# Performance work log

Hardware: AMD Instinct MI355X
Metric: run time of the kernel (lower is better)

Reference implementation:

```python
import jax, jax.numpy as jnp
import numpy as np
from jax import lax

D_MODEL = 64      # feature_dim
D_STATE = 16      # state_dim
D_CONV = 4        # conv_dim
EXPAND = 2
D_INNER = EXPAND * D_MODEL          # 128
DT_RANK = (D_MODEL + 15) // 16      # ceil(d_model/16) = 4, mamba default
IN_DIM = 64
LN_EPS = 1e-3                        # keras LayerNormalization default epsilon


def setup_inputs() -> dict:
    key = jax.random.key(0)
    ks = jax.random.split(key, 12)
    B, L = 16, 8192
    s = 0.02
    x = jax.random.normal(ks[0], (B, L, IN_DIM), jnp.float32)
    W_in = jax.random.normal(ks[1], (IN_DIM, D_MODEL), jnp.float32) * s
    b_in = jnp.zeros((D_MODEL,), jnp.float32)
    in_proj_w = jax.random.normal(ks[2], (D_MODEL, 2 * D_INNER), jnp.float32) * s
    conv_w = jax.random.normal(ks[3], (D_INNER, D_CONV), jnp.float32) * 0.1
    conv_b = jnp.zeros((D_INNER,), jnp.float32)
    x_proj_w = jax.random.normal(ks[4], (D_INNER, DT_RANK + 2 * D_STATE), jnp.float32) * s
    dt_proj_w = jax.random.normal(ks[5], (DT_RANK, D_INNER), jnp.float32) * (DT_RANK ** -0.5)
    # dt bias init so softplus(dt) lands roughly in [dt_min, dt_max]
    dt = jnp.exp(jax.random.uniform(ks[6], (D_INNER,)) * (np.log(0.1) - np.log(0.001)) + np.log(0.001))
    dt_proj_b = dt + jnp.log(-jnp.expm1(-dt))  # inverse softplus
    A_log = jnp.log(jnp.broadcast_to(jnp.arange(1, D_STATE + 1, dtype=jnp.float32), (D_INNER, D_STATE)))
    D_skip = jnp.ones((D_INNER,), jnp.float32)
    out_proj_w = jax.random.normal(ks[7], (D_INNER, D_MODEL), jnp.float32) * s
    ln_gamma = jnp.ones((D_MODEL,), jnp.float32)
    ln_beta = jnp.zeros((D_MODEL,), jnp.float32)
    return {"x": x, "W_in": W_in, "b_in": b_in, "in_proj_w": in_proj_w,
            "conv_w": conv_w, "conv_b": conv_b, "x_proj_w": x_proj_w,
            "dt_proj_w": dt_proj_w, "dt_proj_b": dt_proj_b, "A_log": A_log,
            "D_skip": D_skip, "out_proj_w": out_proj_w,
            "ln_gamma": ln_gamma, "ln_beta": ln_beta}


def reference(x, W_in, b_in, in_proj_w, conv_w, conv_b, x_proj_w,
              dt_proj_w, dt_proj_b, A_log, D_skip, out_proj_w, ln_gamma, ln_beta):
    B, L, _ = x.shape
    # Conv1D kernel_size=1 input projection
    xin = x @ W_in + b_in                          # [B,L,D_MODEL]
    # --- Mamba ---
    xz = xin @ in_proj_w                           # [B,L,2*D_INNER]
    xc, z = xz[..., :D_INNER], xz[..., D_INNER:]
    # causal depthwise conv (groups=d_inner, padding=d_conv-1, crop to L)
    xp = jnp.pad(xc, ((0, 0), (D_CONV - 1, 0), (0, 0)))
    xconv = conv_b
    for k in range(D_CONV):
        xconv = xconv + xp[:, k:k + L, :] * conv_w[:, k]
    u = jax.nn.silu(xconv)                         # [B,L,D_INNER]
    dbc = u @ x_proj_w                             # [B,L,DT_RANK+2*D_STATE]
    dt = jax.nn.softplus(dbc[..., :DT_RANK] @ dt_proj_w + dt_proj_b)   # [B,L,D_INNER]
    Bm = dbc[..., DT_RANK:DT_RANK + D_STATE]       # [B,L,D_STATE]
    Cm = dbc[..., DT_RANK + D_STATE:]              # [B,L,D_STATE]
    A = -jnp.exp(A_log)                            # [D_INNER,D_STATE]

    def step(h, xs):
        dt_t, b_t, c_t, u_t = xs                   # [B,Di],[B,Ds],[B,Ds],[B,Di]
        dA = jnp.exp(dt_t[:, :, None] * A)         # [B,Di,Ds]
        h = dA * h + (dt_t * u_t)[:, :, None] * b_t[:, None, :]
        y = jnp.einsum('bds,bs->bd', h, c_t)
        return h, y

    xs = (jnp.swapaxes(dt, 0, 1), jnp.swapaxes(Bm, 0, 1),
          jnp.swapaxes(Cm, 0, 1), jnp.swapaxes(u, 0, 1))
    h0 = jnp.zeros((B, D_INNER, D_STATE), x.dtype)
    _, ys = lax.scan(step, h0, xs)                 # ys: [L,B,D_INNER]
    y = jnp.swapaxes(ys, 0, 1) + u * D_skip
    y = y * jax.nn.silu(z)
    h_out = y @ out_proj_w                         # [B,L,D_MODEL]
    # residual + LayerNorm
    res = h_out + xin
    mu = jnp.mean(res, axis=-1, keepdims=True)
    var = jnp.mean(jnp.square(res - mu), axis=-1, keepdims=True)
    return ln_gamma * (res - mu) * lax.rsqrt(var + LN_EPS) + ln_beta
```

## Files before the change

kernel.cpp:

```cpp
#include <hip/hip_runtime.h>
#include <hip/hip_bf16.h>
#include <hip/hip_fp16.h>

#define B_SZ   16
#define L_SZ   8192
#define DM     64
#define DI     128
#define NCH    256
#define CLEN   32
#define CH     64
#define RT     80
#define PA     72
#define PU     136
#define PC     132
#define LN_EPS 1e-3f

typedef float  f4 __attribute__((ext_vector_type(4)));
typedef float  f2 __attribute__((ext_vector_type(2)));
typedef short  s8 __attribute__((ext_vector_type(8)));
typedef unsigned short u16;
typedef unsigned int   u32;
#define MFMA16 __builtin_amdgcn_mfma_f32_16x16x32_bf16

__device__ __forceinline__ u16 f2bfu(float f) {
    u32 u = __float_as_uint(f);
    return (u16)((u + 0x7FFFu + ((u >> 16) & 1u)) >> 16);
}
__device__ __forceinline__ u32 pk2bf(float a, float b) {
    return (u32)f2bfu(a) | ((u32)f2bfu(b) << 16);
}
__device__ __forceinline__ float bflo(u32 u) { return __uint_as_float(u << 16); }
__device__ __forceinline__ float bfhi(u32 u) { return __uint_as_float(u & 0xFFFF0000u); }
__device__ __forceinline__ float bfu2f(u16 h) { return __uint_as_float((u32)h << 16); }
__device__ __forceinline__ float h2f(u32 lo16) {
    return __half2float(__ushort_as_half((u16)(lo16 & 0xFFFFu)));
}
__device__ __forceinline__ float fsig(float v) {
    return __builtin_amdgcn_rcpf(1.f + __expf(-v));
}
__device__ __forceinline__ float fsp(float v) {
    return fmaxf(v, 0.f) + __logf(1.f + __expf(-fabsf(v)));
}

__global__ __launch_bounds__(256) void k_prep(
    const float* __restrict__ W_in, const float* __restrict__ in_proj,
    const float* __restrict__ x_proj, const float* __restrict__ Wout,
    u16* __restrict__ Wf1, u16* __restrict__ Wf2,
    u16* __restrict__ Wf3, u16* __restrict__ Wf4)
{
    const int tid = threadIdx.x;
    for (int g = tid; g < 512; g += 256) {
        int lane = g & 63, ks = (g >> 6) & 1, nt = g >> 7;
        int n = nt * 16 + (lane & 15), kb = ks * 32 + (lane >> 4) * 8;
        for (int j = 0; j < 8; j++) Wf1[g * 8 + j] = f2bfu(W_in[(kb + j) * 64 + n]);
    }
    for (int g = tid; g < 2048; g += 256) {
        int lane = g & 63, ks = (g >> 6) & 1, nt = g >> 7;
        int n = nt * 16 + (lane & 15), kb = ks * 32 + (lane >> 4) * 8;
        for (int j = 0; j < 8; j++) Wf2[g * 8 + j] = f2bfu(in_proj[(kb + j) * 256 + n]);
    }
    for (int g = tid; g < 768; g += 256) {
        int lane = g & 63, ks = (g >> 6) & 3, nt = g >> 8;
        int n = nt * 16 + (lane & 15), kb = ks * 32 + (lane >> 4) * 8;
        for (int j = 0; j < 8; j++)
            Wf3[g * 8 + j] = f2bfu(n < 36 ? x_proj[(kb + j) * 36 + n] : 0.f);
    }
    for (int g = tid; g < 1024; g += 256) {
        int lane = g & 63, ks = (g >> 6) & 3, nt = g >> 8;
        int n = nt * 16 + (lane & 15), kb = ks * 32 + (lane >> 4) * 8;
        for (int j = 0; j < 8; j++) Wf4[g * 8 + j] = f2bfu(Wout[(kb + j) * 64 + n]);
    }
}

__global__ __launch_bounds__(256, 4) void k_frontend(
    const float* __restrict__ x, const float* __restrict__ b_in,
    const float* __restrict__ conv_w, const float* __restrict__ conv_b,
    const float* __restrict__ dt_w, const float* __restrict__ dt_b,
    const u16* __restrict__ Wf1, const u16* __restrict__ Wf2, const u16* __restrict__ Wf3,
    const float* __restrict__ A_log,
    float* __restrict__ xin_g, u32* __restrict__ dtu_g,
    float* __restrict__ B_g, float* __restrict__ C_g, u16* __restrict__ sz_g,
    float* __restrict__ hl_ws, float* __restrict__ sdt_ws)
{
    __shared__ __align__(16) char sm[40736];
    u16*   smA   = (u16*)sm;
    u16*   smB   = (u16*)(sm + 11520);
    u16*   smU   = (u16*)sm;
    float* smDtr = (float*)(sm + 17408);
    float* smBf  = (float*)(sm + 18432);
    u16*   smC   = (u16*)(sm + 23040);
    u32*   smDt  = (u32*)(sm + 23040);

    const int tid = threadIdx.x;
    const int w = tid >> 6, lane = tid & 63;
    const int n16 = lane & 15, quad = lane >> 4;
    const int b = blockIdx.y, c0 = blockIdx.x * CH;
    const long long tokbase = (long long)b * L_SZ + c0;

    for (int idx = tid; idx < RT * 16; idx += 256) {
        int r = idx >> 4, c4 = idx & 15;
        int l = c0 - 3 + r;
        float4 v = make_float4(0.f, 0.f, 0.f, 0.f);
        if (r < 67 && l >= 0)
            v = *(const float4*)(x + ((long long)b * L_SZ + l) * 64 + c4 * 4);
        *(uint2*)((char*)smA + r * 144 + c4 * 8) = make_uint2(pk2bf(v.x, v.y), pk2bf(v.z, v.w));
    }
    __syncthreads();

    {
        s8 b0 = *(const s8*)(Wf1 + ((w * 2 + 0) * 64 + lane) * 8);
        s8 b1 = *(const s8*)(Wf1 + ((w * 2 + 1) * 64 + lane) * 8);
        float bias = b_in[w * 16 + n16];
        for (int m = 0; m < 5; m++) {
            int ar = m * 16 + n16;
            s8 a0 = *(const s8*)(smA + ar * PA + quad * 8);
            s8 a1 = *(const s8*)(smA + ar * PA + 32 + quad * 8);
            f4 acc = {0.f, 0.f, 0.f, 0.f};
            acc = MFMA16(a0, b0, acc, 0, 0, 0);
            acc = MFMA16(a1, b1, acc, 0, 0, 0);
#pragma unroll
            for (int reg = 0; reg < 4; reg++) {
                int rr = m * 16 + quad * 4 + reg;
                float v = acc[reg] + bias;
                smB[rr * PA + w * 16 + n16] = f2bfu(v);
                if (rr >= 3 && rr < 67)
                    xin_g[(tokbase + rr - 3) * 64 + w * 16 + n16] = v;
            }
        }
    }
    __syncthreads();

    {
        s8 bf[4][2];
#pragma unroll
        for (int i = 0; i < 4; i++)
#pragma unroll
            for (int ks = 0; ks < 2; ks++)
                bf[i][ks] = *(const s8*)(Wf2 + (((w * 4 + i) * 2 + ks) * 64 + lane) * 8);
        for (int m = 0; m < 5; m++) {
            int ar = m * 16 + n16;
            s8 a0 = *(const s8*)(smB + ar * PA + quad * 8);
            s8 a1 = *(const s8*)(smB + ar * PA + 32 + quad * 8);
#pragma unroll
            for (int i = 0; i < 4; i++) {
                f4 acc = {0.f, 0.f, 0.f, 0.f};
                acc = MFMA16(a0, bf[i][0], acc, 0, 0, 0);
                acc = MFMA16(a1, bf[i][1], acc, 0, 0, 0);
                int cg = (w * 4 + i) * 16 + n16;
#pragma unroll
                for (int reg = 0; reg < 4; reg++) {
                    int rr = m * 16 + quad * 4 + reg;
                    float v = acc[reg];
                    if (cg < 128) {
                        if (rr < 67) {
                            int l = c0 - 3 + rr;
                            smC[rr * PC + cg] = f2bfu(l >= 0 ? v : 0.f);
                        }
                    } else if (rr >= 3 && rr < 67) {
                        sz_g[(tokbase + rr - 3) * 128 + (cg - 128)] = f2bfu(v * fsig(v));
                    }
                }
            }
        }
    }
    __syncthreads();

    {
        const int d2 = lane * 2, ctb = w * 16;
        float4 cw0 = ((const float4*)conv_w)[d2];
        float4 cw1 = ((const float4*)conv_w)[d2 + 1];
        float cb0 = conv_b[d2], cb1 = conv_b[d2 + 1];
        u32 r0 = *(const u32*)((char*)smC + (ctb + 0) * 264 + lane * 4);
        u32 r1 = *(const u32*)((char*)smC + (ctb + 1) * 264 + lane * 4);
        u32 r2 = *(const u32*)((char*)smC + (ctb + 2) * 264 + lane * 4);
#pragma unroll 4
        for (int j = 0; j < 16; j++) {
            int ct = ctb + j;
            u32 r3 = *(const u32*)((char*)smC + (ct + 3) * 264 + lane * 4);
            float v0 = cb0 + bflo(r0) * cw0.x + bflo(r1) * cw0.y + bflo(r2) * cw0.z + bflo(r3) * cw0.w;
            float v1 = cb1 + bfhi(r0) * cw1.x + bfhi(r1) * cw1.y + bfhi(r2) * cw1.z + bfhi(r3) * cw1.w;
            u32 pk = pk2bf(v0 * fsig(v0), v1 * fsig(v1));
            *(u32*)(smU + ct * PU + d2) = pk;
            r0 = r1; r1 = r2; r2 = r3;
        }
    }
    __syncthreads();

    {
        s8 bf3[3][4];
#pragma unroll
        for (int nt = 0; nt < 3; nt++)
#pragma unroll
            for (int ks = 0; ks < 4; ks++)
                bf3[nt][ks] = *(const s8*)(Wf3 + ((nt * 4 + ks) * 64 + lane) * 8);
        f4 acc[3] = {{0.f,0.f,0.f,0.f},{0.f,0.f,0.f,0.f},{0.f,0.f,0.f,0.f}};
        int ar = w * 16 + n16;
#pragma unroll
        for (int ks = 0; ks < 4; ks++) {
            s8 a = *(const s8*)(smU + ar * PU + ks * 32 + quad * 8);
#pragma unroll
            for (int nt = 0; nt < 3; nt++) acc[nt] = MFMA16(a, bf3[nt][ks], acc[nt], 0, 0, 0);
        }
#pragma unroll
        for (int nt = 0; nt < 3; nt++) {
            int c = nt * 16 + n16;
#pragma unroll
            for (int reg = 0; reg < 4; reg++) {
                int rr = w * 16 + quad * 4 + reg;
                float v = acc[nt][reg];
                long long t = tokbase + rr;
                if (c < 4)       smDtr[rr * 4 + c] = v;
                else if (c < 20) { B_g[t * 16 + (c - 4)] = v; smBf[rr * 16 + (c - 4)] = v; }
                else if (c < 36) C_g[t * 16 + (c - 20)] = v;
            }
        }
    }
    __syncthreads();

    {
        const int o2 = lane * 2, grp = w;
        float w00 = dt_w[o2],       w01 = dt_w[o2 + 1];
        float w10 = dt_w[128 + o2], w11 = dt_w[128 + o2 + 1];
        float w20 = dt_w[256 + o2], w21 = dt_w[256 + o2 + 1];
        float w30 = dt_w[384 + o2], w31 = dt_w[384 + o2 + 1];
        float b0 = dt_b[o2], b1 = dt_b[o2 + 1];
#pragma unroll 4
        for (int j = 0; j < 16; j++) {
            int ct = grp * 16 + j;
            float4 q = *(const float4*)(smDtr + ct * 4);
            float v0 = b0 + q.x * w00 + q.y * w10 + q.z * w20 + q.w * w30;
            float v1 = b1 + q.x * w01 + q.y * w11 + q.z * w21 + q.w * w31;
            u32 hpk = (u32)__half_as_ushort(__float2half_rn(fsp(v0))) |
                      ((u32)__half_as_ushort(__float2half_rn(fsp(v1))) << 16);
            smDt[ct * 64 + lane] = hpk;
            u32 upk = *(const u32*)(smU + ct * PU + o2);
            u32 pk0 = (hpk & 0xFFFFu) | (upk << 16);
            u32 pk1 = (hpk >> 16) | (upk & 0xFFFF0000u);
            *(uint2*)(dtu_g + (tokbase + ct) * 128 + o2) = make_uint2(pk0, pk1);
        }
    }
    __syncthreads();

    {
        const int d = tid & 127, cs = tid >> 7;
        const int j2 = d >> 1, hi = d & 1;
        float A[16];
#pragma unroll
        for (int s = 0; s < 16; s++) A[s] = -__expf(A_log[d * 16 + s]);
        const float A0 = A[0];
        bool chain = true;
#pragma unroll
        for (int s = 1; s < 16; s++)
            chain = chain && (fabsf(A[s] - (float)(s + 1) * A0) <= 1e-4f * fabsf(A[s]));

        float sdt = 0.f;
        f2 hh[8];
#pragma unroll
        for (int k = 0; k < 8; k++) hh[k] = f2{0.f, 0.f};

        if (chain) {
            for (int i = 0; i < CLEN; i++) {
                int t = cs * CLEN + i;
                u32 qq = smDt[t * 64 + j2];
                float dtv = __half2float(__ushort_as_half((u16)(hi ? (qq >> 16) : (qq & 0xFFFFu))));
                float uv  = bfu2f(smU[t * PU + d]);
                float duv = dtv * uv;  sdt += dtv;
                f2 du2 = {duv, duv};
                float4 B0 = *(const float4*)(smBf + t * 16);
                float4 B1 = *(const float4*)(smBf + t * 16 + 4);
                float4 B2 = *(const float4*)(smBf + t * 16 + 8);
                float4 B3 = *(const float4*)(smBf + t * 16 + 12);
                f2 bb[8] = {{B0.x,B0.y},{B0.z,B0.w},{B1.x,B1.y},{B1.z,B1.w},
                            {B2.x,B2.y},{B2.z,B2.w},{B3.x,B3.y},{B3.z,B3.w}};
                float p = __expf(dtv * A0);
                float q = p * p, q2v = q * q, q4v = q2v * q2v;
                f2 vq = {q,q}, vq2 = {q2v,q2v}, vq4 = {q4v,q4v};
                f2 m[8];
                m[0] = f2{p, q};
                m[1] = m[0] * vq;  m[2] = m[0] * vq2; m[3] = m[1] * vq2;
                m[4] = m[0] * vq4; m[5] = m[1] * vq4; m[6] = m[2] * vq4; m[7] = m[3] * vq4;
#pragma unroll
                for (int k = 0; k < 8; k++)
                    hh[k] = m[k] * hh[k] + du2 * bb[k];
            }
        } else {
            for (int i = 0; i < CLEN; i++) {
                int t = cs * CLEN + i;
                u32 qq = smDt[t * 64 + j2];
                float dtv = __half2float(__ushort_as_half((u16)(hi ? (qq >> 16) : (qq & 0xFFFFu))));
                float uv  = bfu2f(smU[t * PU + d]);
                float duv = dtv * uv;  sdt += dtv;
                const float* Bp = smBf + t * 16;
#pragma unroll
                for (int k = 0; k < 8; k++) {
                    hh[k].x = __expf(dtv * A[2*k])   * hh[k].x + duv * Bp[2*k];
                    hh[k].y = __expf(dtv * A[2*k+1]) * hh[k].y + duv * Bp[2*k+1];
                }
            }
        }

        const int ch = blockIdx.x * 2 + cs;
        float4* hp4 = (float4*)(hl_ws + (((long long)b * NCH + ch) * 128 + d) * 16);
        hp4[0] = make_float4(hh[0].x, hh[0].y, hh[1].x, hh[1].y);
        hp4[1] = make_float4(hh[2].x, hh[2].y, hh[3].x, hh[3].y);
        hp4[2] = make_float4(hh[4].x, hh[4].y, hh[5].x, hh[5].y);
        hp4[3] = make_float4(hh[6].x, hh[6].y, hh[7].x, hh[7].y);
        sdt_ws[((long long)b * NCH + ch) * 128 + d] = sdt;
    }
}

__global__ __launch_bounds__(256) void k_combine(
    const float* __restrict__ A_log, float* __restrict__ hl_ws,
    const float* __restrict__ sdt_ws)
{
    __shared__ float sH[16 * 16];
    __shared__ float sCT[16];
    const int tid = threadIdx.x;
    const int s = tid & 15, seg = tid >> 4;
    const int bd = blockIdx.x;
    const int b = bd >> 7, d = bd & 127;
    const float A = -__expf(A_log[d * 16 + s]);

    const long long base  = ((long long)b * NCH + seg * 16) * 2048 + d * 16 + s;
    const long long sbase = ((long long)b * NCH + seg * 16) * 128 + d;

    float hinL[16], cum[16];
    float h = 0.f, csum = 0.f;
#pragma unroll
    for (int j = 0; j < 16; j++) {
        float v   = hl_ws[base + (long long)j * 2048];
        float sdt = sdt_ws[sbase + j * 128];
        hinL[j] = h;  cum[j] = csum;
        h = __expf(A * sdt) * h + v;
        csum += sdt;
    }
    sH[seg * 16 + s] = h;
    if (s == 0) sCT[seg] = csum;
    __syncthreads();

    float hseg = 0.f;
    for (int k = 0; k < seg; k++)
        hseg = __expf(A * sCT[k]) * hseg + sH[k * 16 + s];

#pragma unroll
    for (int j = 0; j < 16; j++)
        hl_ws[base + (long long)j * 2048] = hinL[j] + __expf(A * cum[j]) * hseg;
}

__global__ __launch_bounds__(256, 6) void k_backend(
    const u32* __restrict__ dtu_g, const float* __restrict__ B_g,
    const float* __restrict__ C_g, const u16* __restrict__ sz_g,
    const float* __restrict__ A_log, const float* __restrict__ D_skip,
    const float* __restrict__ hin_ws, const float* __restrict__ xin_g,
    const u16* __restrict__ Wf4, const float* __restrict__ gamma,
    const float* __restrict__ beta, float* __restrict__ out)
{
    __shared__ __align__(16) char sm[25600];
    u16*   sy   = (u16*)sm;
    float* smR  = (float*)sm;
    float* sB   = (float*)(sm + 17408);
    float* sC   = (float*)(sm + 21504);

    const int tid = threadIdx.x;
    const int cb = blockIdx.x, b = blockIdx.y;
    const long long tok0 = (long long)b * L_SZ + (long long)cb * 64;

    {
        ((float4*)sB)[tid] = ((const float4*)(B_g + tok0 * 16))[tid];
        ((float4*)sC)[tid] = ((const float4*)(C_g + tok0 * 16))[tid];
    }

    {
        const int d = tid & 127, half = tid >> 7;
        float A[16];
#pragma unroll
        for (int s = 0; s < 16; s++) A[s] = -__expf(A_log[d * 16 + s]);
        const float A0 = A[0];
        bool chain = true;
#pragma unroll
        for (int s = 1; s < 16; s++)
            chain = chain && (fabsf(A[s] - (float)(s + 1) * A0) <= 1e-4f * fabsf(A[s]));

        f2 hh[8];
        {
            const float4* hp = (const float4*)(hin_ws +
                (((long long)b * NCH + 2 * cb + half) * 128 + d) * 16);
            float4 ha = hp[0], hb = hp[1], hc = hp[2], hd = hp[3];
            hh[0] = f2{ha.x, ha.y}; hh[1] = f2{ha.z, ha.w};
            hh[2] = f2{hb.x, hb.y}; hh[3] = f2{hb.z, hb.w};
            hh[4] = f2{hc.x, hc.y}; hh[5] = f2{hc.z, hc.w};
            hh[6] = f2{hd.x, hd.y}; hh[7] = f2{hd.z, hd.w};
        }
        const float Dv = D_skip[d];
        __syncthreads();

        if (chain) {
            for (int i = 0; i < CLEN; i++) {
                int t = half * CLEN + i;
                u32 pk = dtu_g[(tok0 + t) * 128 + d];
                float dtv = h2f(pk);
                float uv  = bfhi(pk);
                float duv = dtv * uv;
                f2 du2 = {duv, duv};
                const float4* Bp = (const float4*)(sB + t * 16);
                float4 B0 = Bp[0], B1 = Bp[1], B2 = Bp[2], B3 = Bp[3];
                const float4* Cp = (const float4*)(sC + t * 16);
                float4 C0 = Cp[0], C1 = Cp[1], C2 = Cp[2], C3 = Cp[3];
                f2 bb[8] = {{B0.x,B0.y},{B0.z,B0.w},{B1.x,B1.y},{B1.z,B1.w},
                            {B2.x,B2.y},{B2.z,B2.w},{B3.x,B3.y},{B3.z,B3.w}};
                f2 cc[8] = {{C0.x,C0.y},{C0.z,C0.w},{C1.x,C1.y},{C1.z,C1.w},
                            {C2.x,C2.y},{C2.z,C2.w},{C3.x,C3.y},{C3.z,C3.w}};
                float p = __expf(dtv * A0);
                float q = p * p, q2v = q * q, q4v = q2v * q2v;
                f2 vq = {q,q}, vq2 = {q2v,q2v}, vq4 = {q4v,q4v};
                f2 m[8];
                m[0] = f2{p, q};
                m[1] = m[0] * vq;  m[2] = m[0] * vq2; m[3] = m[1] * vq2;
                m[4] = m[0] * vq4; m[5] = m[1] * vq4; m[6] = m[2] * vq4; m[7] = m[3] * vq4;
                f2 ys2 = {0.f, 0.f};
#pragma unroll
                for (int k = 0; k < 8; k++) {
                    hh[k] = m[k] * hh[k] + du2 * bb[k];
                    ys2 = hh[k] * cc[k] + ys2;
                }
                float ys = ys2.x + ys2.y;
                float szv = bfu2f(sz_g[(tok0 + t) * 128 + d]);
                sy[t * PU + d] = f2bfu((ys + uv * Dv) * szv);
            }
        } else {
            for (int i = 0; i < CLEN; i++) {
                int t = half * CLEN + i;
                u32 pk = dtu_g[(tok0 + t) * 128 + d];
                float dtv = h2f(pk);
                float uv  = bfhi(pk);
                float duv = dtv * uv;
                const float* Bp = sB + t * 16;
                const float* Cp = sC + t * 16;
                float ys = 0.f;
#pragma unroll
                for (int k = 0; k < 8; k++) {
                    hh[k].x = __expf(dtv * A[2*k])   * hh[k].x + duv * Bp[2*k];
                    hh[k].y = __expf(dtv * A[2*k+1]) * hh[k].y + duv * Bp[2*k+1];
                    ys += hh[k].x * Cp[2*k] + hh[k].y * Cp[2*k+1];
                }
                float szv = bfu2f(sz_g[(tok0 + t) * 128 + d]);
                sy[t * PU + d] = f2bfu((ys + uv * Dv) * szv);
            }
        }
    }
    __syncthreads();

    const int w = tid >> 6, lane = tid & 63;
    const int n16 = lane & 15, quad = lane >> 4;
    f4 accm[4];
    {
        s8 bf[4];
#pragma unroll
        for (int ks = 0; ks < 4; ks++)
            bf[ks] = *(const s8*)(Wf4 + ((w * 4 + ks) * 64 + lane) * 8);
#pragma unroll
        for (int m = 0; m < 4; m++) {
            int ar = m * 16 + n16;
            f4 acc = {0.f, 0.f, 0.f, 0.f};
#pragma unroll
            for (int ks = 0; ks < 4; ks++) {
                s8 a = *(const s8*)(sy + ar * PU + ks * 32 + quad * 8);
                acc = MFMA16(a, bf[ks], acc, 0, 0, 0);
            }
            accm[m] = acc;
        }
    }
    __syncthreads();

    {
#pragma unroll
        for (int m = 0; m < 4; m++)
#pragma unroll
            for (int reg = 0; reg < 4; reg++) {
                int rr = m * 16 + quad * 4 + reg;
                smR[rr * 65 + w * 16 + n16] = accm[m][reg];
            }
    }
    __syncthreads();

    {
        const int row = tid >> 2, part = tid & 3;
        float r[16];
        float s = 0.f, ss = 0.f;
        const float* xr = xin_g + (tok0 + row) * 64 + part * 16;
#pragma unroll
        for (int k = 0; k < 16; k++) {
            float v = smR[row * 65 + part * 16 + k] + xr[k];
            r[k] = v; s += v; ss += v * v;
        }
        s  += __shfl_xor(s, 1, 64);   s  += __shfl_xor(s, 2, 64);
        ss += __shfl_xor(ss, 1, 64);  ss += __shfl_xor(ss, 2, 64);
        float mu  = s * (1.f / 64.f);
        float var = ss * (1.f / 64.f) - mu * mu;
        float rs  = rsqrtf(var + LN_EPS);
        float* orow = out + (tok0 + row) * 64 + part * 16;
        const float* gp = gamma + part * 16;
        const float* bp = beta + part * 16;
#pragma unroll
        for (int k = 0; k < 16; k++)
            orow[k] = gp[k] * (r[k] - mu) * rs + bp[k];
    }
}

extern "C" void kernel_launch(void* const* d_in, const int* in_sizes, int n_in,
                              void* d_out, int out_size, void* d_ws, size_t ws_size,
                              hipStream_t stream)
{
    const float* x       = (const float*)d_in[0];
    const float* W_in    = (const float*)d_in[1];
    const float* b_in    = (const float*)d_in[2];
    const float* in_proj = (const float*)d_in[3];
    const float* conv_w  = (const float*)d_in[4];
    const float* conv_b  = (const float*)d_in[5];
    const float* x_proj  = (const float*)d_in[6];
    const float* dt_w    = (const float*)d_in[7];
    const float* dt_b    = (const float*)d_in[8];
    const float* A_log   = (const float*)d_in[9];
    const float* D_skip  = (const float*)d_in[10];
    const float* Wout    = (const float*)d_in[11];
    const float* gamma   = (const float*)d_in[12];
    const float* beta    = (const float*)d_in[13];
    float* out = (float*)d_out;

    const long long NT = (long long)B_SZ * L_SZ;
    char* ws = (char*)d_ws;
    float*  xin_g = (float*)ws;   ws += NT * 64 * 4;
    u32*    dtu_g = (u32*)ws;     ws += NT * 128 * 4;
    float*  B_g   = (float*)ws;   ws += NT * 16 * 4;
    float*  C_g   = (float*)ws;   ws += NT * 16 * 4;
    u16*    sz_g  = (u16*)ws;     ws += NT * 128 * 2;
    float*  hl_ws  = (float*)ws;  ws += (long long)B_SZ * NCH * 2048 * 4;
    float*  sdt_ws = (float*)ws;  ws += (long long)B_SZ * NCH * 128 * 4;
    u16* Wf1 = (u16*)ws; ws += 4096 * 2;
    u16* Wf2 = (u16*)ws; ws += 16384 * 2;
    u16* Wf3 = (u16*)ws; ws += 6144 * 2;
    u16* Wf4 = (u16*)ws; ws += 8192 * 2;

    k_prep<<<1, 256, 0, stream>>>(W_in, in_proj, x_proj, Wout, Wf1, Wf2, Wf3, Wf4);

    k_frontend<<<dim3(L_SZ / CH, B_SZ), 256, 0, stream>>>(
        x, b_in, conv_w, conv_b, dt_w, dt_b, Wf1, Wf2, Wf3, A_log,
        xin_g, dtu_g, B_g, C_g, sz_g, hl_ws, sdt_ws);

    k_combine<<<B_SZ * 128, 256, 0, stream>>>(A_log, hl_ws, sdt_ws);

    k_backend<<<dim3(L_SZ / 64, B_SZ), 256, 0, stream>>>(
        dtu_g, B_g, C_g, sz_g, A_log, D_skip, hl_ws, xin_g,
        Wf4, gamma, beta, out);
}
```

Before: 257.5 us.

## Shrink frontend LDS by overlapping buffers and rereading dt/u from global

Shared memory for k_frontend drops from about 40KB to 29KB by aliasing the conv input buffer with the A staging area and removing the separate dt buffer. The silu-conv outputs are kept in registers, written to LDS after an extra barrier, and reused when packing dt/u. The chunk scan now reads the packed dt/u values back from the global dtu array, which it just wrote, instead of from LDS. Launch bounds rise to 5 blocks per CU to raise occupancy, at the cost of more register pressure, an extra sync, and global (likely cache-hit) loads in the scan loop.

```diff
diff --git a/kernel.cpp b/kernel.cpp
--- a/kernel.cpp
+++ b/kernel.cpp
@@ -72,7 +72,7 @@
     }
 }
 
-__global__ __launch_bounds__(256, 4) void k_frontend(
+__global__ __launch_bounds__(256, 5) void k_frontend(
     const float* __restrict__ x, const float* __restrict__ b_in,
     const float* __restrict__ conv_w, const float* __restrict__ conv_b,
     const float* __restrict__ dt_w, const float* __restrict__ dt_b,
@@ -82,14 +82,13 @@
     float* __restrict__ B_g, float* __restrict__ C_g, u16* __restrict__ sz_g,
     float* __restrict__ hl_ws, float* __restrict__ sdt_ws)
 {
-    __shared__ __align__(16) char sm[40736];
-    u16*   smA   = (u16*)sm;
-    u16*   smB   = (u16*)(sm + 11520);
+    __shared__ __align__(16) char sm[29216];
+    u16*   smB   = (u16*)sm;
+    u16*   smA   = (u16*)(sm + 11520);
+    u16*   smC   = (u16*)(sm + 11520);
     u16*   smU   = (u16*)sm;
     float* smDtr = (float*)(sm + 17408);
     float* smBf  = (float*)(sm + 18432);
-    u16*   smC   = (u16*)(sm + 23040);
-    u32*   smDt  = (u32*)(sm + 23040);
 
     const int tid = threadIdx.x;
     const int w = tid >> 6, lane = tid & 63;
@@ -165,6 +164,7 @@
     }
     __syncthreads();
 
+    u32 ureg[16];
     {
         const int d2 = lane * 2, ctb = w * 16;
         float4 cw0 = ((const float4*)conv_w)[d2];
@@ -173,16 +173,23 @@
         u32 r0 = *(const u32*)((char*)smC + (ctb + 0) * 264 + lane * 4);
         u32 r1 = *(const u32*)((char*)smC + (ctb + 1) * 264 + lane * 4);
         u32 r2 = *(const u32*)((char*)smC + (ctb + 2) * 264 + lane * 4);
-#pragma unroll 4
+#pragma unroll
         for (int j = 0; j < 16; j++) {
             int ct = ctb + j;
             u32 r3 = *(const u32*)((char*)smC + (ct + 3) * 264 + lane * 4);
             float v0 = cb0 + bflo(r0) * cw0.x + bflo(r1) * cw0.y + bflo(r2) * cw0.z + bflo(r3) * cw0.w;
             float v1 = cb1 + bfhi(r0) * cw1.x + bfhi(r1) * cw1.y + bfhi(r2) * cw1.z + bfhi(r3) * cw1.w;
-            u32 pk = pk2bf(v0 * fsig(v0), v1 * fsig(v1));
-            *(u32*)(smU + ct * PU + d2) = pk;
+            ureg[j] = pk2bf(v0 * fsig(v0), v1 * fsig(v1));
             r0 = r1; r1 = r2; r2 = r3;
         }
+    }
+    __syncthreads();
+
+    {
+        const int d2 = lane * 2, ctb = w * 16;
+#pragma unroll
+        for (int j = 0; j < 16; j++)
+            *(u32*)(smU + (ctb + j) * PU + d2) = ureg[j];
     }
     __syncthreads();
 
@@ -224,18 +231,15 @@
         float w20 = dt_w[256 + o2], w21 = dt_w[256 + o2 + 1];
         float w30 = dt_w[384 + o2], w31 = dt_w[384 + o2 + 1];
         float b0 = dt_b[o2], b1 = dt_b[o2 + 1];
-#pragma unroll 4
+#pragma unroll
         for (int j = 0; j < 16; j++) {
             int ct = grp * 16 + j;
             float4 q = *(const float4*)(smDtr + ct * 4);
             float v0 = b0 + q.x * w00 + q.y * w10 + q.z * w20 + q.w * w30;
             float v1 = b1 + q.x * w01 + q.y * w11 + q.z * w21 + q.w * w31;
-            u32 hpk = (u32)__half_as_ushort(__float2half_rn(fsp(v0))) |
-                      ((u32)__half_as_ushort(__float2half_rn(fsp(v1))) << 16);
-            smDt[ct * 64 + lane] = hpk;
-            u32 upk = *(const u32*)(smU + ct * PU + o2);
-            u32 pk0 = (hpk & 0xFFFFu) | (upk << 16);
-            u32 pk1 = (hpk >> 16) | (upk & 0xFFFF0000u);
+            u32 upk = ureg[j];
+            u32 pk0 = (u32)__half_as_ushort(__float2half_rn(fsp(v0))) | (upk << 16);
+            u32 pk1 = (u32)__half_as_ushort(__float2half_rn(fsp(v1))) | (upk & 0xFFFF0000u);
             *(uint2*)(dtu_g + (tokbase + ct) * 128 + o2) = make_uint2(pk0, pk1);
         }
     }
@@ -243,7 +247,6 @@
 
     {
         const int d = tid & 127, cs = tid >> 7;
-        const int j2 = d >> 1, hi = d & 1;
         float A[16];
 #pragma unroll
         for (int s = 0; s < 16; s++) A[s] = -__expf(A_log[d * 16 + s]);
@@ -261,9 +264,9 @@
         if (chain) {
             for (int i = 0; i < CLEN; i++) {
                 int t = cs * CLEN + i;
-                u32 qq = smDt[t * 64 + j2];
-                float dtv = __half2float(__ushort_as_half((u16)(hi ? (qq >> 16) : (qq & 0xFFFFu))));
-                float uv  = bfu2f(smU[t * PU + d]);
+                u32 pk = dtu_g[(tokbase + t) * 128 + d];
+                float dtv = h2f(pk);
+                float uv  = bfhi(pk);
                 float duv = dtv * uv;  sdt += dtv;
                 f2 du2 = {duv, duv};
                 float4 B0 = *(const float4*)(smBf + t * 16);
@@ -286,9 +289,9 @@
         } else {
             for (int i = 0; i < CLEN; i++) {
                 int t = cs * CLEN + i;
-                u32 qq = smDt[t * 64 + j2];
-                float dtv = __half2float(__ushort_as_half((u16)(hi ? (qq >> 16) : (qq & 0xFFFFu))));
-                float uv  = bfu2f(smU[t * PU + d]);
+                u32 pk = dtu_g[(tokbase + t) * 128 + d];
+                float dtv = h2f(pk);
+                float uv  = bfhi(pk);
                 float duv = dtv * uv;  sdt += dtv;
                 const float* Bp = smBf + t * 16;
 #pragma unroll
```

Measured after the change: 285.5 us. +10.9%, slower.
